# Performance work log

Measured on AMD Instinct MI355X. Metric: run time of the kernel, lower is better.

## Reference

```python
import jax, jax.numpy as jnp
import numpy as np


def setup_inputs() -> dict:
    key = jax.random.key(0)
    k1, k2, k3, k4 = jax.random.split(key, 4)
    L, d, n_tokens = 4096, 2048, 4096
    x = jax.random.normal(k1, (L, d), dtype=jnp.float32)
    Wq_w = jax.random.normal(k2, (d, d), dtype=jnp.float32) * (1.0 / np.sqrt(d))
    Pk = jax.random.normal(k3, (1, n_tokens, d), dtype=jnp.float32)
    Pv = jax.random.normal(k4, (1, n_tokens, d), dtype=jnp.float32)
    return {"x": x, "Wq_w": Wq_w, "Pk": Pk, "Pv": Pv, "sliding_window_size": 1024}


def reference(x, Wq_w, Pk, Pv, sliding_window_size):
    # x: (L, d); Pk/Pv: (1, n_tokens, d). Single-head cross attention to a
    # fixed parameter token bank with a bidirectional sliding-window mask
    # |q_idx - kv_idx| < sliding_window_size (flex_attention semantics,
    # default scale = 1/sqrt(d)).
    L, d = x.shape
    n_tokens = Pk.shape[1]
    scale = 1.0 / np.sqrt(d).astype(np.float32)

    q = x @ Wq_w.T                                    # (L, d)
    scores = jnp.einsum('ld,td->lt', q, Pk[0]) * scale  # (L, n_tokens)

    q_idx = jnp.arange(L)[:, None]
    kv_idx = jnp.arange(n_tokens)[None, :]
    mask = jnp.abs(q_idx - kv_idx) < sliding_window_size  # (L, n_tokens)

    neg_inf = jnp.asarray(jnp.finfo(scores.dtype).min, scores.dtype)
    probs = jax.nn.softmax(jnp.where(mask, scores, neg_inf), axis=-1)
    y = jnp.einsum('lt,td->ld', probs, Pv[0])         # (L, d)
    return y[None, :, :]                              # (1, L, d) after squeeze(1)
```

## Files before the change

### kernel.cpp

```cpp
#include <hip/hip_runtime.h>


using bf16x8 = __attribute__((ext_vector_type(8))) short;
using f32x4  = __attribute__((ext_vector_type(4))) float;

#define LDIM 4096
#define TDIM 4096
#define DDIM 2048

static __device__ __forceinline__ unsigned short f2bf(float f) {
  union { float f; unsigned u; } c; c.f = f;
  unsigned r = c.u + 0x7FFFu + ((c.u >> 16) & 1u);
  return (unsigned short)(r >> 16);
}
static __device__ __forceinline__ unsigned pack2(float a, float b) {
  return (unsigned)f2bf(a) | ((unsigned)f2bf(b) << 16);
}
static __device__ __forceinline__ void gload16(const void* g, void* l) {
  __builtin_amdgcn_global_load_lds((const __attribute__((address_space(1))) void*)g,
                                   (__attribute__((address_space(3))) void*)l, 16, 0, 0);
}

__global__ __launch_bounds__(256) void k_prep(const float* __restrict__ x,
                                              const float* __restrict__ Wq,
                                              const float* __restrict__ Pk,
                                              const float* __restrict__ Pv,
                                              unsigned short* __restrict__ xb,
                                              unsigned short* __restrict__ wb,
                                              unsigned short* __restrict__ kb,
                                              unsigned short* __restrict__ vt,
                                              float* __restrict__ rowsum) {
  const int tid = threadIdx.x;
  const int b = blockIdx.x;
  if (b < 10240) {
    const float* in; unsigned short* out; size_t i;
    if (b < 4096)      { in = x;  out = xb; i = (size_t)b * 256 + tid; }
    else if (b < 6144) { in = Wq; out = wb; i = (size_t)(b - 4096) * 256 + tid; }
    else               { in = Pk; out = kb; i = (size_t)(b - 6144) * 256 + tid; }
    const float4* p = (const float4*)(in + i * 8);
    float4 a = p[0], c = p[1];
    uint4 o = { pack2(a.x, a.y), pack2(a.z, a.w), pack2(c.x, c.y), pack2(c.z, c.w) };
    *(uint4*)(out + i * 8) = o;
    return;
  }
  if (b == 12288) {
    for (int k = tid; k < LDIM; k += 256) rowsum[k] = 0.f;
    return;
  }
  __shared__ unsigned short tile[64][72];
  const int b2 = b - 10240;
  const int t0 = (b2 & 63) * 64, j0 = (b2 >> 6) * 64;
  const int r = tid >> 4, c4 = (tid & 15) * 4;
#pragma unroll
  for (int rr = 0; rr < 64; rr += 16) {
    float4 v = *(const float4*)(Pv + (size_t)(t0 + r + rr) * DDIM + j0 + c4);
    tile[c4 + 0][r + rr] = f2bf(v.x);
    tile[c4 + 1][r + rr] = f2bf(v.y);
    tile[c4 + 2][r + rr] = f2bf(v.z);
    tile[c4 + 3][r + rr] = f2bf(v.w);
  }
  __syncthreads();
  const int jr = tid >> 3, tc = (tid & 7) * 8;
#pragma unroll
  for (int jj = 0; jj < 64; jj += 32)
    *(uint4*)(vt + (size_t)(j0 + jr + jj) * TDIM + t0 + tc) =
        *(const uint4*)&tile[jr + jj][tc];
}

static __device__ __forceinline__ void gemm_loop(const unsigned short* __restrict__ A,
                                                 const unsigned short* __restrict__ B,
                                                 int m0, int n0, long lda, long ldb,
                                                 int kbeg, int kend,
                                                 unsigned short* As, unsigned short* Bs,
                                                 f32x4 (&acc)[4][2]) {
  const int tid = threadIdx.x;
  const int wave = tid >> 6, lane = tid & 63;
  const int quad = lane >> 4, l16 = lane & 15;
  const int wm = wave >> 2, wn = wave & 3;
  const int srow = wave * 16 + (lane >> 3);
  const int scb  = (lane & 7) ^ (lane >> 3);

  const unsigned short* gA = A + (long)(m0 + srow) * lda + scb * 8;
  const unsigned short* gB = B + (long)(n0 + srow) * ldb + scb * 8;
  unsigned short* lA = As + wave * 1024;
  unsigned short* lB = Bs + wave * 1024;

  const int sw = (l16 & 7) * 8;

  for (int k0 = kbeg; k0 < kend; k0 += 64) {
    gload16(gA + k0,           lA);
    gload16(gA + k0 + 8 * lda, lA + 512);
    gload16(gB + k0,           lB);
    gload16(gB + k0 + 8 * ldb, lB + 512);
    __syncthreads();
    bf16x8 af[4][2], bfr[2][2];
#pragma unroll
    for (int i = 0; i < 4; i++)
#pragma unroll
      for (int h = 0; h < 2; h++)
        af[i][h] = *(const bf16x8*)&As[(wm * 64 + i * 16 + l16) * 64 +
                                       (((h * 4 + quad) * 8) ^ sw)];
#pragma unroll
    for (int j = 0; j < 2; j++)
#pragma unroll
      for (int h = 0; h < 2; h++)
        bfr[j][h] = *(const bf16x8*)&Bs[(wn * 32 + j * 16 + l16) * 64 +
                                        (((h * 4 + quad) * 8) ^ sw)];
#pragma unroll
    for (int h = 0; h < 2; h++)
#pragma unroll
      for (int i = 0; i < 4; i++)
#pragma unroll
        for (int j = 0; j < 2; j++)
          acc[i][j] = __builtin_amdgcn_mfma_f32_16x16x32_bf16(af[i][h], bfr[j][h],
                                                              acc[i][j], 0, 0, 0);
    __syncthreads();
  }
}

static __device__ __forceinline__ void gemm_loop_n64(const unsigned short* __restrict__ A,
                                                     const unsigned short* __restrict__ B,
                                                     int m0, int n0, long lda, long ldb,
                                                     int kbeg, int kend,
                                                     unsigned short* As, unsigned short* Bs,
                                                     f32x4 (&acc)[2][2]) {
  const int tid = threadIdx.x;
  const int wave = tid >> 6, lane = tid & 63;
  const int quad = lane >> 4, l16 = lane & 15;
  const int wm = wave >> 1, wn = wave & 1;
  const int arow = wave * 16 + (lane >> 3);
  const int brow = wave * 8 + (lane >> 3);
  const int scb  = (lane & 7) ^ (lane >> 3);

  const unsigned short* gA = A + (long)(m0 + arow) * lda + scb * 8;
  const unsigned short* gB = B + (long)(n0 + brow) * ldb + scb * 8;
  unsigned short* lA = As + wave * 1024;
  unsigned short* lB = Bs + wave * 512;

  const int sw = (l16 & 7) * 8;

  for (int k0 = kbeg; k0 < kend; k0 += 64) {
    gload16(gA + k0,           lA);
    gload16(gA + k0 + 8 * lda, lA + 512);
    gload16(gB + k0,           lB);
    __syncthreads();
    bf16x8 af[2][2], bfr[2][2];
#pragma unroll
    for (int i = 0; i < 2; i++)
#pragma unroll
      for (int h = 0; h < 2; h++)
        af[i][h] = *(const bf16x8*)&As[(wm * 32 + i * 16 + l16) * 64 +
                                       (((h * 4 + quad) * 8) ^ sw)];
#pragma unroll
    for (int j = 0; j < 2; j++)
#pragma unroll
      for (int h = 0; h < 2; h++)
        bfr[j][h] = *(const bf16x8*)&Bs[(wn * 32 + j * 16 + l16) * 64 +
                                        (((h * 4 + quad) * 8) ^ sw)];
#pragma unroll
    for (int h = 0; h < 2; h++)
#pragma unroll
      for (int i = 0; i < 2; i++)
#pragma unroll
        for (int j = 0; j < 2; j++)
          acc[i][j] = __builtin_amdgcn_mfma_f32_16x16x32_bf16(af[i][h], bfr[j][h],
                                                              acc[i][j], 0, 0, 0);
    __syncthreads();
  }
}

__global__ __launch_bounds__(512, 8) void k1_qgemm(const unsigned short* __restrict__ X,
                                                   const unsigned short* __restrict__ W,
                                                   unsigned short* __restrict__ q) {
  __shared__ __align__(16) unsigned short As[128 * 64];
  __shared__ __align__(16) unsigned short Bs[64 * 64];
  const unsigned flat = blockIdx.y * 32 + blockIdx.x;
  const unsigned swz = (flat & 7) * 128 + (flat >> 3);
  const int bx = swz & 31, by = swz >> 5;
  f32x4 acc[2][2] = {};
  const int m0 = by * 128, n0 = bx * 64;
  gemm_loop_n64(X, W, m0, n0, DDIM, DDIM, 0, DDIM, As, Bs, acc);
  const int tid = threadIdx.x;
  const int wave = tid >> 6, lane = tid & 63;
  const int quad = lane >> 4, l16 = lane & 15, wm = wave >> 1, wn = wave & 1;
#pragma unroll
  for (int i = 0; i < 2; i++)
#pragma unroll
    for (int j = 0; j < 2; j++)
#pragma unroll
      for (int r = 0; r < 4; r++) {
        int row = m0 + wm * 32 + i * 16 + quad * 4 + r;
        int col = n0 + wn * 32 + j * 16 + l16;
        q[(long)row * DDIM + col] = f2bf(acc[i][j][r]);
      }
}

__global__ __launch_bounds__(512) void k2_qk(const unsigned short* __restrict__ Q,
                                             const unsigned short* __restrict__ Kb,
                                             unsigned short* __restrict__ P,
                                             float* __restrict__ rowsum,
                                             const int* __restrict__ wptr) {
  const unsigned flat = blockIdx.y * 32 + blockIdx.x;
  const unsigned swz = (flat & 7) * 128 + (flat >> 3);
  const int bx = swz & 31, by = swz >> 5;
  const int w = *wptr;
  const int l0 = by * 128, t0 = bx * 128;
  int lo = l0 - w + 1; if (lo < 0) lo = 0;
  int hi = l0 + 127 + w - 1; if (hi > TDIM - 1) hi = TDIM - 1;
  if (bx < (lo >> 7) || bx > (hi >> 7)) return;
  __shared__ __align__(16) unsigned short As[128 * 64];
  __shared__ __align__(16) unsigned short Bs[128 * 64];
  f32x4 acc[4][2] = {};
  gemm_loop(Q, Kb, l0, t0, DDIM, DDIM, 0, DDIM, As, Bs, acc);
  const float scale = 0.022097086912079608f;
  const int tid = threadIdx.x;
  const int wave = tid >> 6, lane = tid & 63;
  const int quad = lane >> 4, l16 = lane & 15, wm = wave >> 2, wn = wave & 3;
#pragma unroll
  for (int i = 0; i < 4; i++) {
    float rs[4] = {0.f, 0.f, 0.f, 0.f};
#pragma unroll
    for (int j = 0; j < 2; j++)
#pragma unroll
      for (int r = 0; r < 4; r++) {
        int l = l0 + wm * 64 + i * 16 + quad * 4 + r;
        int t = t0 + wn * 32 + j * 16 + l16;
        int dlt = l - t; dlt = dlt < 0 ? -dlt : dlt;
        float e = 0.f;
        if (dlt < w) e = __expf(acc[i][j][r] * scale);
        unsigned short bv = f2bf(e);
        P[(long)l * TDIM + t] = bv;
        rs[r] += __uint_as_float((unsigned)bv << 16);
      }
#pragma unroll
    for (int r = 0; r < 4; ++r) {
      float s = rs[r];
      s += __shfl_xor(s, 1);
      s += __shfl_xor(s, 2);
      s += __shfl_xor(s, 4);
      s += __shfl_xor(s, 8);
      if (l16 == 0) atomicAdd(&rowsum[l0 + wm * 64 + i * 16 + quad * 4 + r], s);
    }
  }
}

__global__ __launch_bounds__(512, 8) void k3_pv(const unsigned short* __restrict__ P,
                                                const unsigned short* __restrict__ Vt,
                                                const float* __restrict__ rowsum,
                                                float* __restrict__ Y,
                                                const int* __restrict__ wptr) {
  const unsigned flat = blockIdx.y * 32 + blockIdx.x;
  const unsigned swz = (flat & 7) * 128 + (flat >> 3);
  const int bx = swz & 31, by = swz >> 5;
  const int w = *wptr;
  const int l0 = by * 128, j0 = bx * 64;
  int lo = l0 - w + 1; if (lo < 0) lo = 0;
  int hi = l0 + 127 + w - 1; if (hi > TDIM - 1) hi = TDIM - 1;
  const int kb = (lo >> 7) * 128, ke = ((hi >> 7) + 1) * 128;
  __shared__ __align__(16) unsigned short As[128 * 64];
  __shared__ __align__(16) unsigned short Bs[64 * 64];
  f32x4 acc[2][2] = {};
  gemm_loop_n64(P, Vt, l0, j0, TDIM, TDIM, kb, ke, As, Bs, acc);
  const int tid = threadIdx.x;
  const int wave = tid >> 6, lane = tid & 63;
  const int quad = lane >> 4, l16 = lane & 15, wm = wave >> 1, wn = wave & 1;
#pragma unroll
  for (int i = 0; i < 2; i++)
#pragma unroll
    for (int r = 0; r < 4; r++) {
      const int l = l0 + wm * 32 + i * 16 + quad * 4 + r;
      const float inv = 1.0f / rowsum[l];
#pragma unroll
      for (int j = 0; j < 2; j++)
        Y[(long)l * DDIM + j0 + wn * 32 + j * 16 + l16] = acc[i][j][r] * inv;
    }
}

extern "C" void kernel_launch(void* const* d_in, const int* in_sizes, int n_in,
                              void* d_out, int out_size, void* d_ws, size_t ws_size,
                              hipStream_t stream) {
  const float* x  = (const float*)d_in[0];
  const float* Wq = (const float*)d_in[1];
  const float* Pk = (const float*)d_in[2];
  const float* Pv = (const float*)d_in[3];
  const int* wptr = (const int*)d_in[4];
  float* Y = (float*)d_out;

  unsigned short* base = (unsigned short*)d_ws;
  unsigned short* Pm = base;
  unsigned short* xb = base;
  unsigned short* wb = base + (size_t)LDIM * DDIM;
  unsigned short* kb = base + (size_t)TDIM * TDIM;
  unsigned short* vt = kb + (size_t)TDIM * DDIM;
  unsigned short* qb = vt + (size_t)DDIM * TDIM;
  float* rowsum = (float*)(qb + (size_t)LDIM * DDIM);

  k_prep<<<12289, 256, 0, stream>>>(x, Wq, Pk, Pv, xb, wb, kb, vt, rowsum);
  k1_qgemm<<<dim3(DDIM / 64, LDIM / 128), 512, 0, stream>>>(xb, wb, qb);
  k2_qk<<<dim3(TDIM / 128, LDIM / 128), 512, 0, stream>>>(qb, kb, Pm, rowsum, wptr);
  k3_pv<<<dim3(DDIM / 64, LDIM / 128), 512, 0, stream>>>(Pm, vt, rowsum, Y, wptr);
}
```

Before: 301.2 us.

## Use 128x128 tiles with 1024-thread blocks for Q and PV GEMMs, drop block swizzle

The Q-projection and PV GEMMs move from 128x64 tiles on 512-thread blocks to 128x128 tiles on 1024-thread blocks (16 waves, each computing 32x32). Each wave now issues one A and one B async LDS load per k-step. This halves the number of blocks and doubles the reuse of each A tile across the N dimension. The L2-friendly block-index swizzle is removed from all three GEMM kernels in favour of plain grid order, which may reduce cache locality. The 1024-thread blocks also limit per-CU occupancy and add more waves to each barrier.

```diff
diff --git a/kernel.cpp b/kernel.cpp
--- a/kernel.cpp
+++ b/kernel.cpp
@@ -67,12 +67,12 @@
         *(const uint4*)&tile[jr + jj][tc];
 }
 
-static __device__ __forceinline__ void gemm_loop(const unsigned short* __restrict__ A,
-                                                 const unsigned short* __restrict__ B,
-                                                 int m0, int n0, long lda, long ldb,
-                                                 int kbeg, int kend,
-                                                 unsigned short* As, unsigned short* Bs,
-                                                 f32x4 (&acc)[4][2]) {
+static __device__ __forceinline__ void gemm_loop8(const unsigned short* __restrict__ A,
+                                                  const unsigned short* __restrict__ B,
+                                                  int m0, int n0, long lda, long ldb,
+                                                  int kbeg, int kend,
+                                                  unsigned short* As, unsigned short* Bs,
+                                                  f32x4 (&acc)[4][2]) {
   const int tid = threadIdx.x;
   const int wave = tid >> 6, lane = tid & 63;
   const int quad = lane >> 4, l16 = lane & 15;
@@ -118,31 +118,29 @@
   }
 }
 
-static __device__ __forceinline__ void gemm_loop_n64(const unsigned short* __restrict__ A,
-                                                     const unsigned short* __restrict__ B,
-                                                     int m0, int n0, long lda, long ldb,
-                                                     int kbeg, int kend,
-                                                     unsigned short* As, unsigned short* Bs,
-                                                     f32x4 (&acc)[2][2]) {
+static __device__ __forceinline__ void gemm_loop16(const unsigned short* __restrict__ A,
+                                                   const unsigned short* __restrict__ B,
+                                                   int m0, int n0, long lda, long ldb,
+                                                   int kbeg, int kend,
+                                                   unsigned short* As, unsigned short* Bs,
+                                                   f32x4 (&acc)[2][2]) {
   const int tid = threadIdx.x;
   const int wave = tid >> 6, lane = tid & 63;
   const int quad = lane >> 4, l16 = lane & 15;
-  const int wm = wave >> 1, wn = wave & 1;
-  const int arow = wave * 16 + (lane >> 3);
-  const int brow = wave * 8 + (lane >> 3);
+  const int wm = wave >> 2, wn = wave & 3;
+  const int srow = wave * 8 + (lane >> 3);
   const int scb  = (lane & 7) ^ (lane >> 3);
 
-  const unsigned short* gA = A + (long)(m0 + arow) * lda + scb * 8;
-  const unsigned short* gB = B + (long)(n0 + brow) * ldb + scb * 8;
-  unsigned short* lA = As + wave * 1024;
+  const unsigned short* gA = A + (long)(m0 + srow) * lda + scb * 8;
+  const unsigned short* gB = B + (long)(n0 + srow) * ldb + scb * 8;
+  unsigned short* lA = As + wave * 512;
   unsigned short* lB = Bs + wave * 512;
 
   const int sw = (l16 & 7) * 8;
 
   for (int k0 = kbeg; k0 < kend; k0 += 64) {
-    gload16(gA + k0,           lA);
-    gload16(gA + k0 + 8 * lda, lA + 512);
-    gload16(gB + k0,           lB);
+    gload16(gA + k0, lA);
+    gload16(gB + k0, lB);
     __syncthreads();
     bf16x8 af[2][2], bfr[2][2];
 #pragma unroll
@@ -169,20 +167,17 @@
   }
 }
 
-__global__ __launch_bounds__(512, 8) void k1_qgemm(const unsigned short* __restrict__ X,
-                                                   const unsigned short* __restrict__ W,
-                                                   unsigned short* __restrict__ q) {
+__global__ __launch_bounds__(1024, 8) void k1_qgemm(const unsigned short* __restrict__ X,
+                                                    const unsigned short* __restrict__ W,
+                                                    unsigned short* __restrict__ q) {
   __shared__ __align__(16) unsigned short As[128 * 64];
-  __shared__ __align__(16) unsigned short Bs[64 * 64];
-  const unsigned flat = blockIdx.y * 32 + blockIdx.x;
-  const unsigned swz = (flat & 7) * 128 + (flat >> 3);
-  const int bx = swz & 31, by = swz >> 5;
+  __shared__ __align__(16) unsigned short Bs[128 * 64];
   f32x4 acc[2][2] = {};
-  const int m0 = by * 128, n0 = bx * 64;
-  gemm_loop_n64(X, W, m0, n0, DDIM, DDIM, 0, DDIM, As, Bs, acc);
-  const int tid = threadIdx.x;
-  const int wave = tid >> 6, lane = tid & 63;
-  const int quad = lane >> 4, l16 = lane & 15, wm = wave >> 1, wn = wave & 1;
+  const int m0 = blockIdx.y * 128, n0 = blockIdx.x * 128;
+  gemm_loop16(X, W, m0, n0, DDIM, DDIM, 0, DDIM, As, Bs, acc);
+  const int tid = threadIdx.x;
+  const int wave = tid >> 6, lane = tid & 63;
+  const int quad = lane >> 4, l16 = lane & 15, wm = wave >> 2, wn = wave & 3;
 #pragma unroll
   for (int i = 0; i < 2; i++)
 #pragma unroll
@@ -200,18 +195,15 @@
                                              unsigned short* __restrict__ P,
                                              float* __restrict__ rowsum,
                                              const int* __restrict__ wptr) {
-  const unsigned flat = blockIdx.y * 32 + blockIdx.x;
-  const unsigned swz = (flat & 7) * 128 + (flat >> 3);
-  const int bx = swz & 31, by = swz >> 5;
   const int w = *wptr;
-  const int l0 = by * 128, t0 = bx * 128;
+  const int l0 = blockIdx.y * 128, t0 = blockIdx.x * 128;
   int lo = l0 - w + 1; if (lo < 0) lo = 0;
   int hi = l0 + 127 + w - 1; if (hi > TDIM - 1) hi = TDIM - 1;
-  if (bx < (lo >> 7) || bx > (hi >> 7)) return;
+  if ((int)blockIdx.x < (lo >> 7) || (int)blockIdx.x > (hi >> 7)) return;
   __shared__ __align__(16) unsigned short As[128 * 64];
   __shared__ __align__(16) unsigned short Bs[128 * 64];
   f32x4 acc[4][2] = {};
-  gemm_loop(Q, Kb, l0, t0, DDIM, DDIM, 0, DDIM, As, Bs, acc);
+  gemm_loop8(Q, Kb, l0, t0, DDIM, DDIM, 0, DDIM, As, Bs, acc);
   const float scale = 0.022097086912079608f;
   const int tid = threadIdx.x;
   const int wave = tid >> 6, lane = tid & 63;
@@ -244,26 +236,23 @@
   }
 }
 
-__global__ __launch_bounds__(512, 8) void k3_pv(const unsigned short* __restrict__ P,
-                                                const unsigned short* __restrict__ Vt,
-                                                const float* __restrict__ rowsum,
-                                                float* __restrict__ Y,
-                                                const int* __restrict__ wptr) {
-  const unsigned flat = blockIdx.y * 32 + blockIdx.x;
-  const unsigned swz = (flat & 7) * 128 + (flat >> 3);
-  const int bx = swz & 31, by = swz >> 5;
+__global__ __launch_bounds__(1024, 8) void k3_pv(const unsigned short* __restrict__ P,
+                                                 const unsigned short* __restrict__ Vt,
+                                                 const float* __restrict__ rowsum,
+                                                 float* __restrict__ Y,
+                                                 const int* __restrict__ wptr) {
   const int w = *wptr;
-  const int l0 = by * 128, j0 = bx * 64;
+  const int l0 = blockIdx.y * 128, j0 = blockIdx.x * 128;
   int lo = l0 - w + 1; if (lo < 0) lo = 0;
   int hi = l0 + 127 + w - 1; if (hi > TDIM - 1) hi = TDIM - 1;
   const int kb = (lo >> 7) * 128, ke = ((hi >> 7) + 1) * 128;
   __shared__ __align__(16) unsigned short As[128 * 64];
-  __shared__ __align__(16) unsigned short Bs[64 * 64];
+  __shared__ __align__(16) unsigned short Bs[128 * 64];
   f32x4 acc[2][2] = {};
-  gemm_loop_n64(P, Vt, l0, j0, TDIM, TDIM, kb, ke, As, Bs, acc);
-  const int tid = threadIdx.x;
-  const int wave = tid >> 6, lane = tid & 63;
-  const int quad = lane >> 4, l16 = lane & 15, wm = wave >> 1, wn = wave & 1;
+  gemm_loop16(P, Vt, l0, j0, TDIM, TDIM, kb, ke, As, Bs, acc);
+  const int tid = threadIdx.x;
+  const int wave = tid >> 6, lane = tid & 63;
+  const int quad = lane >> 4, l16 = lane & 15, wm = wave >> 2, wn = wave & 3;
 #pragma unroll
   for (int i = 0; i < 2; i++)
 #pragma unroll
@@ -296,7 +285,7 @@
   float* rowsum = (float*)(qb + (size_t)LDIM * DDIM);
 
   k_prep<<<12289, 256, 0, stream>>>(x, Wq, Pk, Pv, xb, wb, kb, vt, rowsum);
-  k1_qgemm<<<dim3(DDIM / 64, LDIM / 128), 512, 0, stream>>>(xb, wb, qb);
+  k1_qgemm<<<dim3(DDIM / 128, LDIM / 128), 1024, 0, stream>>>(xb, wb, qb);
   k2_qk<<<dim3(TDIM / 128, LDIM / 128), 512, 0, stream>>>(qb, kb, Pm, rowsum, wptr);
-  k3_pv<<<dim3(DDIM / 64, LDIM / 128), 512, 0, stream>>>(Pm, vt, rowsum, Y, wptr);
-}
+  k3_pv<<<dim3(DDIM / 128, LDIM / 128), 1024, 0, stream>>>(Pm, vt, rowsum, Y, wptr);
+}
```

Measured after the change: 283.9 us. 5.7% less time.
